# Kernel optimization log

Measured on AMD Instinct MI355X. Metric: run time of the kernel, lower is better.

Reference implementation:

```python
import jax, jax.numpy as jnp
import numpy as np

NUM_USERS = 50000
NUM_ITEMS = 50000
N = NUM_USERS + NUM_ITEMS
EMBED_K = 64
N_LAYERS = 3
FEAT = 2048
N_EDGES = 2000000
BATCH = 8192
LEAKY_SLOPE = 0.2


def _l2norm(x):
    # torch F.normalize(p=2, dim=1): x / max(||x||, 1e-12)
    return x / jnp.maximum(jnp.linalg.norm(x, axis=1, keepdims=True), 1e-12)


def setup_inputs():
    key = jax.random.key(0)
    ks = jax.random.split(key, 12)
    s = 1.0 / np.sqrt(EMBED_K)
    return {
        "Gu": jax.random.normal(ks[0], (NUM_USERS, EMBED_K), jnp.float32) * 0.1,
        "Gi": jax.random.normal(ks[1], (NUM_ITEMS, EMBED_K), jnp.float32) * 0.1,
        "Tu": jax.random.normal(ks[2], (NUM_USERS, EMBED_K), jnp.float32) * 0.1,
        "F": jax.random.uniform(ks[3], (NUM_ITEMS, FEAT), jnp.float32),
        "proj_w": jax.random.normal(ks[4], (EMBED_K, FEAT), jnp.float32) / np.sqrt(FEAT),
        "proj_b": jnp.zeros((EMBED_K,), jnp.float32),
        "W1": jax.random.normal(ks[5], (N_LAYERS, EMBED_K, EMBED_K), jnp.float32) * s,
        "b1": jnp.zeros((N_LAYERS, EMBED_K), jnp.float32),
        "W2": jax.random.normal(ks[6], (N_LAYERS, EMBED_K, EMBED_K), jnp.float32) * s,
        "b2": jnp.zeros((N_LAYERS, EMBED_K), jnp.float32),
        "edge_weight": jax.random.uniform(ks[7], (N_EDGES,), jnp.float32) * 0.05,
        "edge_index": jax.random.randint(ks[8], (2, N_EDGES), 0, N, jnp.int32),
        "users": jax.random.randint(ks[9], (BATCH,), 0, NUM_USERS, jnp.int32),
        "items": jax.random.randint(ks[10], (BATCH,), 0, NUM_ITEMS, jnp.int32),
    }


def _propagate(Gu, Gi, W1, b1, W2, b2, edge_weight, edge_index):
    src, dst = edge_index[0], edge_index[1]
    x = jnp.concatenate([Gu, Gi], axis=0)  # [N, d]
    embs = [x]
    for l in range(N_LAYERS):
        # sparse adjacency aggregation: agg = A_hat @ x
        msg = x[src] * edge_weight[:, None]              # [E, d]
        agg = jax.ops.segment_sum(msg, dst, num_segments=N)  # [N, d]
        # NGCF layer: W1(x + agg) + W2(x * agg), leaky relu
        h = (x + agg) @ W1[l].T + b1[l] + (x * agg) @ W2[l].T + b2[l]
        h = jax.nn.leaky_relu(h, LEAKY_SLOPE)
        # dropout p=0 (identity), then per-node L2 normalize
        h = _l2norm(h)
        embs.append(h)
        x = h
    all_e = jnp.mean(jnp.stack(embs, axis=1), axis=1)  # mean over layers
    return all_e[:NUM_USERS], all_e[NUM_USERS:]


def reference(Gu, Gi, Tu, F, proj_w, proj_b, W1, b1, W2, b2, edge_weight, edge_index, users, items):
    gu, gi = _propagate(Gu, Gi, W1, b1, W2, b2, edge_weight, edge_index)
    gamma_u = gu[users]          # [B, d]
    gamma_i = gi[items]          # [B, d]
    theta_u = Tu[users]          # [B, d]
    proj_i = _l2norm(F[items] @ proj_w.T + proj_b)  # [B, d]
    xui = jnp.sum(gamma_u * gamma_i, axis=1) + jnp.sum(theta_u * proj_i, axis=1)
    return xui
```

## Files before the change

kernel.cpp:

```cpp
#include <hip/hip_runtime.h>

#define NUSERS 50000
#define NITEMS 50000
#define NN (NUSERS + NITEMS)
#define KDIM 64
#define NLAYERS 3
#define FEAT 2048
#define NEDGES 2000000
#define BATCH 8192
#define SLOPE 0.2f

#define BSLOT 64
#define CNT_PAD 100352
#define XBLK 6250
#define CBLK 98
#define TBLK 128
#define NNK (NN * KDIM)
#define PROJ_BLOCKS (BATCH / 16)
#define FILL_BLOCKS ((NEDGES + 511) / 512)

typedef __attribute__((ext_vector_type(8))) short bf16x8;
typedef __attribute__((ext_vector_type(4))) float f32x4;

union U8 {
    bf16x8 v;
    uint4 u;
};

__device__ __forceinline__ unsigned short f2bf(float f) {
    unsigned int u = __float_as_uint(f);
    unsigned int r = (u + 0x7fffu + ((u >> 16) & 1u)) >> 16;
    return (unsigned short)r;
}
__device__ __forceinline__ unsigned int pack2(float a, float b) {
    return (unsigned int)f2bf(a) | ((unsigned int)f2bf(b) << 16);
}
__device__ __forceinline__ float b2f(unsigned short h) {
    return __uint_as_float((unsigned int)h << 16);
}

__global__ __launch_bounds__(256) void setup_kernel(const float* __restrict__ Gu,
                                                    const float* __restrict__ Gi,
                                                    const float* __restrict__ pw,
                                                    unsigned short* __restrict__ xh,
                                                    int* __restrict__ cnt,
                                                    unsigned short* __restrict__ pwh) {
    int bx = blockIdx.x;
    if (bx < XBLK) {
        int i = bx * 256 + threadIdx.x;
        const int totalU = NUSERS * KDIM / 4;
        float4 v = (i < totalU) ? ((const float4*)Gu)[i] : ((const float4*)Gi)[i - totalU];
        ushort4 h;
        h.x = f2bf(v.x); h.y = f2bf(v.y); h.z = f2bf(v.z); h.w = f2bf(v.w);
        ((ushort4*)xh)[i] = h;
    } else if (bx < XBLK + CBLK) {
        int i = (bx - XBLK) * 256 + threadIdx.x;
        ((int4*)cnt)[i] = make_int4(0, 0, 0, 0);
    } else {
        int i = (bx - XBLK - CBLK) * 256 + threadIdx.x;
        float4 v = ((const float4*)pw)[i];
        ushort4 h;
        h.x = f2bf(v.x); h.y = f2bf(v.y); h.z = f2bf(v.z); h.w = f2bf(v.w);
        ((ushort4*)pwh)[i] = h;
    }
}

__global__ __launch_bounds__(512) void proj_fill_kernel(const float* __restrict__ F,
                                                        const unsigned short* __restrict__ pwh,
                                                        const float* __restrict__ pb,
                                                        const int* __restrict__ items,
                                                        float* __restrict__ projB,
                                                        const int* __restrict__ ei,
                                                        const float* __restrict__ ew,
                                                        int* __restrict__ cnt,
                                                        unsigned int* __restrict__ bucket) {
    __shared__ float lds[8][64][16];
    int t = threadIdx.x;
    if (blockIdx.x >= PROJ_BLOCKS) {
        int e = (blockIdx.x - PROJ_BLOCKS) * 512 + t;
        if (e < NEDGES) {
            int src = ei[e];
            int dst = ei[NEDGES + e];
            int slot = atomicAdd(&cnt[dst], 1);
            if (slot < BSLOT)
                bucket[((long long)dst << 6) + slot] =
                    ((unsigned int)src << 15) | ((unsigned int)f2bf(ew[e]) & 0x7FFFu);
        }
        return;
    }
    int l = t & 63, w = t >> 6, m16 = l & 15, g4 = l >> 4;
    int i0 = blockIdx.x * 16;
    int item = items[i0 + m16];
    const float* frow = F + (long long)item * FEAT + g4 * 8;
    f32x4 acc[4];
#pragma unroll
    for (int c = 0; c < 4; ++c) acc[c] = (f32x4){0.f, 0.f, 0.f, 0.f};
    float4 fa[8], fb[8];
#pragma unroll
    for (int u = 0; u < 8; ++u) {
        const float* p = frow + (w * 8 + u) * 32;
        fa[u] = *(const float4*)p;
        fb[u] = *(const float4*)(p + 4);
    }
#pragma unroll
    for (int u = 0; u < 8; ++u) {
        U8 af;
        af.u = make_uint4(pack2(fa[u].x, fa[u].y), pack2(fa[u].z, fa[u].w),
                          pack2(fb[u].x, fb[u].y), pack2(fb[u].z, fb[u].w));
#pragma unroll
        for (int c = 0; c < 4; ++c) {
            bf16x8 bw = *(const bf16x8*)(pwh + (long long)(c * 16 + m16) * FEAT +
                                         (w * 8 + u) * 32 + g4 * 8);
            acc[c] = __builtin_amdgcn_mfma_f32_16x16x32_bf16(af.v, bw, acc[c], 0, 0, 0);
        }
    }
#pragma unroll
    for (int c = 0; c < 4; ++c)
#pragma unroll
        for (int reg = 0; reg < 4; ++reg) lds[w][l][c * 4 + reg] = acc[c][reg];
    __syncthreads();
    for (int e = t; e < 1024; e += 512) {
        int ll = e >> 4, v = e & 15;
        float s = lds[0][ll][v];
#pragma unroll
        for (int ww = 1; ww < 8; ++ww) s += lds[ww][ll][v];
        lds[0][ll][v] = s;
    }
    __syncthreads();
    if (w == 0) {
        float av[4][4];
        float sq[4] = {0.f, 0.f, 0.f, 0.f};
#pragma unroll
        for (int c = 0; c < 4; ++c) {
            float bb = pb[c * 16 + m16];
#pragma unroll
            for (int reg = 0; reg < 4; ++reg) {
                float h = lds[0][l][c * 4 + reg] + bb;
                av[c][reg] = h;
                sq[reg] += h * h;
            }
        }
#pragma unroll
        for (int reg = 0; reg < 4; ++reg) {
#pragma unroll
            for (int off = 1; off < 16; off <<= 1) sq[reg] += __shfl_xor(sq[reg], off);
            sq[reg] = 1.0f / fmaxf(sqrtf(sq[reg]), 1e-12f);
        }
#pragma unroll
        for (int reg = 0; reg < 4; ++reg) {
            int b = i0 + g4 * 4 + reg;
#pragma unroll
            for (int c = 0; c < 4; ++c)
                projB[(long long)b * KDIM + c * 16 + m16] = av[c][reg] * sq[reg];
        }
    }
}

__global__ __launch_bounds__(256) void agg_kernel(const unsigned short* __restrict__ xh,
                                                  const unsigned int* __restrict__ bucket,
                                                  const int* __restrict__ cnt,
                                                  unsigned short* __restrict__ aggh) {
    int t = threadIdx.x;
    int lane = t & 63, wid = t >> 6;
    int g = lane >> 3, l8 = lane & 7;
    int n = (blockIdx.x * 4 + wid) * 8 + g;
    if (n >= NN) return;
    int m = cnt[n];
    if (m > BSLOT) m = BSLOT;
    const unsigned int* bk = bucket + ((long long)n << 6);
    const uint4* x4 = (const uint4*)xh;
    float a0[8], a1[8], a2[8], a3[8];
#pragma unroll
    for (int q = 0; q < 8; ++q) { a0[q] = 0.f; a1[q] = 0.f; a2[q] = 0.f; a3[q] = 0.f; }
    int j = 0;
    for (; j + 4 <= m; j += 4) {
        unsigned int p0 = bk[j], p1 = bk[j + 1], p2 = bk[j + 2], p3 = bk[j + 3];
        uint4 u0 = x4[((long long)(p0 >> 15) << 3) + l8];
        uint4 u1 = x4[((long long)(p1 >> 15) << 3) + l8];
        uint4 u2 = x4[((long long)(p2 >> 15) << 3) + l8];
        uint4 u3 = x4[((long long)(p3 >> 15) << 3) + l8];
        float w0 = __uint_as_float((p0 & 0x7FFFu) << 16);
        float w1 = __uint_as_float((p1 & 0x7FFFu) << 16);
        float w2 = __uint_as_float((p2 & 0x7FFFu) << 16);
        float w3 = __uint_as_float((p3 & 0x7FFFu) << 16);
        a0[0] += w0 * __uint_as_float(u0.x << 16); a0[1] += w0 * __uint_as_float(u0.x & 0xFFFF0000u);
        a0[2] += w0 * __uint_as_float(u0.y << 16); a0[3] += w0 * __uint_as_float(u0.y & 0xFFFF0000u);
        a0[4] += w0 * __uint_as_float(u0.z << 16); a0[5] += w0 * __uint_as_float(u0.z & 0xFFFF0000u);
        a0[6] += w0 * __uint_as_float(u0.w << 16); a0[7] += w0 * __uint_as_float(u0.w & 0xFFFF0000u);
        a1[0] += w1 * __uint_as_float(u1.x << 16); a1[1] += w1 * __uint_as_float(u1.x & 0xFFFF0000u);
        a1[2] += w1 * __uint_as_float(u1.y << 16); a1[3] += w1 * __uint_as_float(u1.y & 0xFFFF0000u);
        a1[4] += w1 * __uint_as_float(u1.z << 16); a1[5] += w1 * __uint_as_float(u1.z & 0xFFFF0000u);
        a1[6] += w1 * __uint_as_float(u1.w << 16); a1[7] += w1 * __uint_as_float(u1.w & 0xFFFF0000u);
        a2[0] += w2 * __uint_as_float(u2.x << 16); a2[1] += w2 * __uint_as_float(u2.x & 0xFFFF0000u);
        a2[2] += w2 * __uint_as_float(u2.y << 16); a2[3] += w2 * __uint_as_float(u2.y & 0xFFFF0000u);
        a2[4] += w2 * __uint_as_float(u2.z << 16); a2[5] += w2 * __uint_as_float(u2.z & 0xFFFF0000u);
        a2[6] += w2 * __uint_as_float(u2.w << 16); a2[7] += w2 * __uint_as_float(u2.w & 0xFFFF0000u);
        a3[0] += w3 * __uint_as_float(u3.x << 16); a3[1] += w3 * __uint_as_float(u3.x & 0xFFFF0000u);
        a3[2] += w3 * __uint_as_float(u3.y << 16); a3[3] += w3 * __uint_as_float(u3.y & 0xFFFF0000u);
        a3[4] += w3 * __uint_as_float(u3.z << 16); a3[5] += w3 * __uint_as_float(u3.z & 0xFFFF0000u);
        a3[6] += w3 * __uint_as_float(u3.w << 16); a3[7] += w3 * __uint_as_float(u3.w & 0xFFFF0000u);
    }
    for (; j < m; ++j) {
        unsigned int p0 = bk[j];
        uint4 u0 = x4[((long long)(p0 >> 15) << 3) + l8];
        float w0 = __uint_as_float((p0 & 0x7FFFu) << 16);
        a0[0] += w0 * __uint_as_float(u0.x << 16); a0[1] += w0 * __uint_as_float(u0.x & 0xFFFF0000u);
        a0[2] += w0 * __uint_as_float(u0.y << 16); a0[3] += w0 * __uint_as_float(u0.y & 0xFFFF0000u);
        a0[4] += w0 * __uint_as_float(u0.z << 16); a0[5] += w0 * __uint_as_float(u0.z & 0xFFFF0000u);
        a0[6] += w0 * __uint_as_float(u0.w << 16); a0[7] += w0 * __uint_as_float(u0.w & 0xFFFF0000u);
    }
#pragma unroll
    for (int q = 0; q < 8; ++q) a0[q] = (a0[q] + a1[q]) + (a2[q] + a3[q]);
    uint4 o;
    o.x = pack2(a0[0], a0[1]); o.y = pack2(a0[2], a0[3]);
    o.z = pack2(a0[4], a0[5]); o.w = pack2(a0[6], a0[7]);
    *(uint4*)(aggh + (long long)n * KDIM + l8 * 8) = o;
}

__global__ __launch_bounds__(256) void gemm_layer_kernel(const unsigned short* __restrict__ xh_in,
                                                         const unsigned short* __restrict__ aggh,
                                                         const float* __restrict__ W1,
                                                         const float* __restrict__ b1,
                                                         const float* __restrict__ W2,
                                                         const float* __restrict__ b2,
                                                         unsigned short* __restrict__ xhout,
                                                         int layer) {
    __shared__ unsigned short sS[64 * 72];
    __shared__ unsigned short sP[64 * 72];
    __shared__ unsigned short sW1[64 * 72];
    __shared__ unsigned short sW2[64 * 72];
    int t = threadIdx.x;
    const float* W1g = W1 + (long long)layer * KDIM * KDIM;
    const float* W2g = W2 + (long long)layer * KDIM * KDIM;
    for (int idx = t; idx < KDIM * KDIM; idx += 256) {
        int j = idx >> 6, k = idx & 63;
        sW1[j * 72 + k] = f2bf(W1g[idx]);
        sW2[j * 72 + k] = f2bf(W2g[idx]);
    }
    int n0 = blockIdx.x * 64;
    {
        int r = t >> 2, q = t & 3;
        int node = n0 + r;
        unsigned short* dS = &sS[r * 72 + q * 16];
        unsigned short* dP = &sP[r * 72 + q * 16];
        if (node < NN) {
            const unsigned short* xb = xh_in + (long long)node * KDIM + q * 16;
            const unsigned short* ab = aggh + (long long)node * KDIM + q * 16;
            uint4 hx = *(const uint4*)xb;
            uint4 hx2 = *(const uint4*)(xb + 8);
            uint4 ha = *(const uint4*)ab;
            uint4 ha2 = *(const uint4*)(ab + 8);
            uint4 swv, pwv, swv2, pwv2;
#define PROC(XW, AW, SW, PW)                                                        \
            {                                                                       \
                float xx0 = __uint_as_float((XW) << 16);                            \
                float xx1 = __uint_as_float((XW) & 0xFFFF0000u);                    \
                float aa0 = __uint_as_float((AW) << 16);                            \
                float aa1 = __uint_as_float((AW) & 0xFFFF0000u);                    \
                SW = pack2(xx0 + aa0, xx1 + aa1);                                   \
                PW = pack2(xx0 * aa0, xx1 * aa1);                                   \
            }
            PROC(hx.x, ha.x, swv.x, pwv.x)
            PROC(hx.y, ha.y, swv.y, pwv.y)
            PROC(hx.z, ha.z, swv.z, pwv.z)
            PROC(hx.w, ha.w, swv.w, pwv.w)
            PROC(hx2.x, ha2.x, swv2.x, pwv2.x)
            PROC(hx2.y, ha2.y, swv2.y, pwv2.y)
            PROC(hx2.z, ha2.z, swv2.z, pwv2.z)
            PROC(hx2.w, ha2.w, swv2.w, pwv2.w)
#undef PROC
            *(uint4*)dS = swv;
            *(uint4*)(dS + 8) = swv2;
            *(uint4*)dP = pwv;
            *(uint4*)(dP + 8) = pwv2;
        } else {
            uint4 z = make_uint4(0, 0, 0, 0);
            *(uint4*)dS = z; *(uint4*)(dS + 8) = z;
            *(uint4*)dP = z; *(uint4*)(dP + 8) = z;
        }
    }
    __syncthreads();

    int l = t & 63, w = t >> 6, m16 = l & 15, g4 = l >> 4;
    f32x4 acc[4];
#pragma unroll
    for (int c = 0; c < 4; ++c) {
        float bb = b1[layer * KDIM + c * 16 + m16] + b2[layer * KDIM + c * 16 + m16];
        acc[c] = (f32x4){bb, bb, bb, bb};
    }
    const int abase = (w * 16 + m16) * 72;
#pragma unroll
    for (int kh = 0; kh < 2; ++kh) {
        int ko = kh * 32 + g4 * 8;
        bf16x8 aS = *(const bf16x8*)&sS[abase + ko];
        bf16x8 aP = *(const bf16x8*)&sP[abase + ko];
#pragma unroll
        for (int c = 0; c < 4; ++c) {
            bf16x8 bw1 = *(const bf16x8*)&sW1[(c * 16 + m16) * 72 + ko];
            acc[c] = __builtin_amdgcn_mfma_f32_16x16x32_bf16(aS, bw1, acc[c], 0, 0, 0);
            bf16x8 bw2 = *(const bf16x8*)&sW2[(c * 16 + m16) * 72 + ko];
            acc[c] = __builtin_amdgcn_mfma_f32_16x16x32_bf16(aP, bw2, acc[c], 0, 0, 0);
        }
    }

    float sq[4] = {0.f, 0.f, 0.f, 0.f};
#pragma unroll
    for (int c = 0; c < 4; ++c) {
#pragma unroll
        for (int reg = 0; reg < 4; ++reg) {
            float h = acc[c][reg];
            h = h > 0.f ? h : SLOPE * h;
            acc[c][reg] = h;
            sq[reg] += h * h;
        }
    }
#pragma unroll
    for (int reg = 0; reg < 4; ++reg) {
#pragma unroll
        for (int off = 1; off < 16; off <<= 1) sq[reg] += __shfl_xor(sq[reg], off);
        sq[reg] = 1.0f / fmaxf(sqrtf(sq[reg]), 1e-12f);
    }
#pragma unroll
    for (int reg = 0; reg < 4; ++reg) {
        int node = n0 + w * 16 + g4 * 4 + reg;
        if (node < NN) {
#pragma unroll
            for (int c = 0; c < 4; ++c)
                xhout[(long long)node * KDIM + c * 16 + m16] = f2bf(acc[c][reg] * sq[reg]);
        }
    }
}

__global__ __launch_bounds__(256) void final_kernel(const unsigned short* __restrict__ xh0,
                                                    const unsigned short* __restrict__ xh1,
                                                    const unsigned short* __restrict__ xh2,
                                                    const unsigned short* __restrict__ xh3,
                                                    const float* __restrict__ Tu,
                                                    const float* __restrict__ projB,
                                                    const int* __restrict__ users,
                                                    const int* __restrict__ items,
                                                    float* __restrict__ out) {
    int lane = threadIdx.x & 63;
    int wid = threadIdx.x >> 6;
    int b = blockIdx.x * 4 + wid;
    if (b >= BATCH) return;
    int u = users[b];
    int it = NUSERS + items[b];
    long long uo = (long long)u * KDIM + lane;
    long long io = (long long)it * KDIM + lane;
    float gu = b2f(xh0[uo]) + b2f(xh1[uo]) + b2f(xh2[uo]) + b2f(xh3[uo]);
    float gi = b2f(xh0[io]) + b2f(xh1[io]) + b2f(xh2[io]) + b2f(xh3[io]);
    float tu = Tu[(long long)u * KDIM + lane];
    float pi = projB[(long long)b * KDIM + lane];
    float v = gu * gi * (1.0f / 16.0f) + tu * pi;
#pragma unroll
    for (int off = 32; off > 0; off >>= 1) v += __shfl_xor(v, off);
    if (lane == 0) out[b] = v;
}

extern "C" void kernel_launch(void* const* d_in, const int* in_sizes, int n_in,
                              void* d_out, int out_size, void* d_ws, size_t ws_size,
                              hipStream_t stream) {
    const float* Gu = (const float*)d_in[0];
    const float* Gi = (const float*)d_in[1];
    const float* Tu = (const float*)d_in[2];
    const float* F = (const float*)d_in[3];
    const float* pw = (const float*)d_in[4];
    const float* pb = (const float*)d_in[5];
    const float* W1 = (const float*)d_in[6];
    const float* b1 = (const float*)d_in[7];
    const float* W2 = (const float*)d_in[8];
    const float* b2 = (const float*)d_in[9];
    const float* ew = (const float*)d_in[10];
    const int* ei = (const int*)d_in[11];
    const int* users = (const int*)d_in[12];
    const int* items = (const int*)d_in[13];
    float* out = (float*)d_out;

    float* projB = (float*)d_ws;
    unsigned int* bucket = (unsigned int*)(projB + (size_t)BATCH * KDIM);
    int* cnt = (int*)(bucket + (size_t)NN * BSLOT);
    unsigned short* aggh = (unsigned short*)(cnt + CNT_PAD);
    unsigned short* pwh = aggh + (size_t)NNK;
    unsigned short* xh0 = pwh + (size_t)KDIM * FEAT;
    unsigned short* xh1 = xh0 + (size_t)NNK;
    unsigned short* xh2 = xh1 + (size_t)NNK;
    unsigned short* xh3 = xh2 + (size_t)NNK;

    setup_kernel<<<XBLK + CBLK + TBLK, 256, 0, stream>>>(Gu, Gi, pw, xh0, cnt, pwh);
    proj_fill_kernel<<<PROJ_BLOCKS + FILL_BLOCKS, 512, 0, stream>>>(F, pwh, pb, items, projB,
                                                                    ei, ew, cnt, bucket);

    unsigned short* xs[4] = {xh0, xh1, xh2, xh3};
    for (int ll = 0; ll < NLAYERS; ++ll) {
        agg_kernel<<<(NN + 31) / 32, 256, 0, stream>>>(xs[ll], bucket, cnt, aggh);
        gemm_layer_kernel<<<(NN + 63) / 64, 256, 0, stream>>>(xs[ll], aggh, W1, b1, W2, b2,
                                                              xs[ll + 1], ll);
    }

    final_kernel<<<BATCH / 4, 256, 0, stream>>>(xh0, xh1, xh2, xh3, Tu, projB, users, items, out);
}
```

Measured before the change: 333.8 us.

## Fuse sparse aggregation with NGCF layer GEMM and pre-convert weights to bf16

Merges agg_kernel and gemm_layer_kernel into one per-layer kernel. Each lane gathers neighbour rows directly into the MFMA A-operand layout (node per m16, k-slice per g4), so the intermediate aggregate buffer is no longer written to and re-read from global memory, and two launches per layer are removed. W1/W2 are converted to bf16 once in the setup kernel and read from global memory instead of being staged through LDS in every block. The trade-off is a less contiguous gather (each lane loads two 16-byte chunks per neighbour) and divergence from differing node degrees within a wave.

```diff
diff --git a/kernel.cpp b/kernel.cpp
--- a/kernel.cpp
+++ b/kernel.cpp
@@ -15,6 +15,7 @@
 #define XBLK 6250
 #define CBLK 98
 #define TBLK 128
+#define W4BLK 12
 #define NNK (NN * KDIM)
 #define PROJ_BLOCKS (BATCH / 16)
 #define FILL_BLOCKS ((NEDGES + 511) / 512)
@@ -39,12 +40,39 @@
     return __uint_as_float((unsigned int)h << 16);
 }
 
+#define ACC8(A, W, U)                                   \
+    A[0] += (W) * __uint_as_float((U).x << 16);         \
+    A[1] += (W) * __uint_as_float((U).x & 0xFFFF0000u); \
+    A[2] += (W) * __uint_as_float((U).y << 16);         \
+    A[3] += (W) * __uint_as_float((U).y & 0xFFFF0000u); \
+    A[4] += (W) * __uint_as_float((U).z << 16);         \
+    A[5] += (W) * __uint_as_float((U).z & 0xFFFF0000u); \
+    A[6] += (W) * __uint_as_float((U).w << 16);         \
+    A[7] += (W) * __uint_as_float((U).w & 0xFFFF0000u);
+
+#define MKSP(XV, A, SU, PU)                                                          \
+    {                                                                                \
+        float x0, x1;                                                                \
+        x0 = __uint_as_float((XV).x << 16); x1 = __uint_as_float((XV).x & 0xFFFF0000u); \
+        (SU).x = pack2(x0 + (A)[0], x1 + (A)[1]); (PU).x = pack2(x0 * (A)[0], x1 * (A)[1]); \
+        x0 = __uint_as_float((XV).y << 16); x1 = __uint_as_float((XV).y & 0xFFFF0000u); \
+        (SU).y = pack2(x0 + (A)[2], x1 + (A)[3]); (PU).y = pack2(x0 * (A)[2], x1 * (A)[3]); \
+        x0 = __uint_as_float((XV).z << 16); x1 = __uint_as_float((XV).z & 0xFFFF0000u); \
+        (SU).z = pack2(x0 + (A)[4], x1 + (A)[5]); (PU).z = pack2(x0 * (A)[4], x1 * (A)[5]); \
+        x0 = __uint_as_float((XV).w << 16); x1 = __uint_as_float((XV).w & 0xFFFF0000u); \
+        (SU).w = pack2(x0 + (A)[6], x1 + (A)[7]); (PU).w = pack2(x0 * (A)[6], x1 * (A)[7]); \
+    }
+
 __global__ __launch_bounds__(256) void setup_kernel(const float* __restrict__ Gu,
                                                     const float* __restrict__ Gi,
                                                     const float* __restrict__ pw,
+                                                    const float* __restrict__ W1,
+                                                    const float* __restrict__ W2,
                                                     unsigned short* __restrict__ xh,
                                                     int* __restrict__ cnt,
-                                                    unsigned short* __restrict__ pwh) {
+                                                    unsigned short* __restrict__ pwh,
+                                                    unsigned short* __restrict__ w1h,
+                                                    unsigned short* __restrict__ w2h) {
     int bx = blockIdx.x;
     if (bx < XBLK) {
         int i = bx * 256 + threadIdx.x;
@@ -56,12 +84,21 @@
     } else if (bx < XBLK + CBLK) {
         int i = (bx - XBLK) * 256 + threadIdx.x;
         ((int4*)cnt)[i] = make_int4(0, 0, 0, 0);
-    } else {
+    } else if (bx < XBLK + CBLK + TBLK) {
         int i = (bx - XBLK - CBLK) * 256 + threadIdx.x;
         float4 v = ((const float4*)pw)[i];
         ushort4 h;
         h.x = f2bf(v.x); h.y = f2bf(v.y); h.z = f2bf(v.z); h.w = f2bf(v.w);
         ((ushort4*)pwh)[i] = h;
+    } else {
+        int b2x = bx - XBLK - CBLK - TBLK;
+        const float* srcw = (b2x < W4BLK) ? W1 : W2;
+        unsigned short* dstw = (b2x < W4BLK) ? w1h : w2h;
+        int i = (b2x % W4BLK) * 256 + threadIdx.x;
+        float4 v = ((const float4*)srcw)[i];
+        ushort4 h;
+        h.x = f2bf(v.x); h.y = f2bf(v.y); h.z = f2bf(v.z); h.w = f2bf(v.w);
+        ((ushort4*)dstw)[i] = h;
     }
 }
 
@@ -156,151 +193,82 @@
     }
 }
 
-__global__ __launch_bounds__(256) void agg_kernel(const unsigned short* __restrict__ xh,
-                                                  const unsigned int* __restrict__ bucket,
-                                                  const int* __restrict__ cnt,
-                                                  unsigned short* __restrict__ aggh) {
+__global__ __launch_bounds__(256) void layer_fused_kernel(const unsigned short* __restrict__ xh_in,
+                                                          const unsigned int* __restrict__ bucket,
+                                                          const int* __restrict__ cnt,
+                                                          const unsigned short* __restrict__ w1h,
+                                                          const unsigned short* __restrict__ w2h,
+                                                          const float* __restrict__ b1,
+                                                          const float* __restrict__ b2,
+                                                          unsigned short* __restrict__ xhout,
+                                                          int layer) {
     int t = threadIdx.x;
-    int lane = t & 63, wid = t >> 6;
-    int g = lane >> 3, l8 = lane & 7;
-    int n = (blockIdx.x * 4 + wid) * 8 + g;
-    if (n >= NN) return;
-    int m = cnt[n];
+    int l = t & 63, w = t >> 6;
+    int m16 = l & 15, g4 = l >> 4;
+    int node = blockIdx.x * 64 + w * 16 + m16;
+    int ok = node < NN;
+    int nc = ok ? node : 0;
+    int m = ok ? cnt[nc] : 0;
     if (m > BSLOT) m = BSLOT;
-    const unsigned int* bk = bucket + ((long long)n << 6);
-    const uint4* x4 = (const uint4*)xh;
-    float a0[8], a1[8], a2[8], a3[8];
-#pragma unroll
-    for (int q = 0; q < 8; ++q) { a0[q] = 0.f; a1[q] = 0.f; a2[q] = 0.f; a3[q] = 0.f; }
+    const unsigned int* bk = bucket + ((long long)nc << 6);
+    const uint4* x4 = (const uint4*)xh_in;
+
+    float a0l[8], a0h[8], a1l[8], a1h[8];
+#pragma unroll
+    for (int q = 0; q < 8; ++q) { a0l[q] = 0.f; a0h[q] = 0.f; a1l[q] = 0.f; a1h[q] = 0.f; }
     int j = 0;
-    for (; j + 4 <= m; j += 4) {
-        unsigned int p0 = bk[j], p1 = bk[j + 1], p2 = bk[j + 2], p3 = bk[j + 3];
-        uint4 u0 = x4[((long long)(p0 >> 15) << 3) + l8];
-        uint4 u1 = x4[((long long)(p1 >> 15) << 3) + l8];
-        uint4 u2 = x4[((long long)(p2 >> 15) << 3) + l8];
-        uint4 u3 = x4[((long long)(p3 >> 15) << 3) + l8];
+    for (; j + 2 <= m; j += 2) {
+        unsigned int p0 = bk[j], p1 = bk[j + 1];
+        long long r0 = (long long)(p0 >> 15) << 3;
+        long long r1 = (long long)(p1 >> 15) << 3;
+        uint4 u0l = x4[r0 + g4];
+        uint4 u0h = x4[r0 + 4 + g4];
+        uint4 u1l = x4[r1 + g4];
+        uint4 u1h = x4[r1 + 4 + g4];
         float w0 = __uint_as_float((p0 & 0x7FFFu) << 16);
         float w1 = __uint_as_float((p1 & 0x7FFFu) << 16);
-        float w2 = __uint_as_float((p2 & 0x7FFFu) << 16);
-        float w3 = __uint_as_float((p3 & 0x7FFFu) << 16);
-        a0[0] += w0 * __uint_as_float(u0.x << 16); a0[1] += w0 * __uint_as_float(u0.x & 0xFFFF0000u);
-        a0[2] += w0 * __uint_as_float(u0.y << 16); a0[3] += w0 * __uint_as_float(u0.y & 0xFFFF0000u);
-        a0[4] += w0 * __uint_as_float(u0.z << 16); a0[5] += w0 * __uint_as_float(u0.z & 0xFFFF0000u);
-        a0[6] += w0 * __uint_as_float(u0.w << 16); a0[7] += w0 * __uint_as_float(u0.w & 0xFFFF0000u);
-        a1[0] += w1 * __uint_as_float(u1.x << 16); a1[1] += w1 * __uint_as_float(u1.x & 0xFFFF0000u);
-        a1[2] += w1 * __uint_as_float(u1.y << 16); a1[3] += w1 * __uint_as_float(u1.y & 0xFFFF0000u);
-        a1[4] += w1 * __uint_as_float(u1.z << 16); a1[5] += w1 * __uint_as_float(u1.z & 0xFFFF0000u);
-        a1[6] += w1 * __uint_as_float(u1.w << 16); a1[7] += w1 * __uint_as_float(u1.w & 0xFFFF0000u);
-        a2[0] += w2 * __uint_as_float(u2.x << 16); a2[1] += w2 * __uint_as_float(u2.x & 0xFFFF0000u);
-        a2[2] += w2 * __uint_as_float(u2.y << 16); a2[3] += w2 * __uint_as_float(u2.y & 0xFFFF0000u);
-        a2[4] += w2 * __uint_as_float(u2.z << 16); a2[5] += w2 * __uint_as_float(u2.z & 0xFFFF0000u);
-        a2[6] += w2 * __uint_as_float(u2.w << 16); a2[7] += w2 * __uint_as_float(u2.w & 0xFFFF0000u);
-        a3[0] += w3 * __uint_as_float(u3.x << 16); a3[1] += w3 * __uint_as_float(u3.x & 0xFFFF0000u);
-        a3[2] += w3 * __uint_as_float(u3.y << 16); a3[3] += w3 * __uint_as_float(u3.y & 0xFFFF0000u);
-        a3[4] += w3 * __uint_as_float(u3.z << 16); a3[5] += w3 * __uint_as_float(u3.z & 0xFFFF0000u);
-        a3[6] += w3 * __uint_as_float(u3.w << 16); a3[7] += w3 * __uint_as_float(u3.w & 0xFFFF0000u);
-    }
-    for (; j < m; ++j) {
+        ACC8(a0l, w0, u0l)
+        ACC8(a0h, w0, u0h)
+        ACC8(a1l, w1, u1l)
+        ACC8(a1h, w1, u1h)
+    }
+    if (j < m) {
         unsigned int p0 = bk[j];
-        uint4 u0 = x4[((long long)(p0 >> 15) << 3) + l8];
+        long long r0 = (long long)(p0 >> 15) << 3;
+        uint4 u0l = x4[r0 + g4];
+        uint4 u0h = x4[r0 + 4 + g4];
         float w0 = __uint_as_float((p0 & 0x7FFFu) << 16);
-        a0[0] += w0 * __uint_as_float(u0.x << 16); a0[1] += w0 * __uint_as_float(u0.x & 0xFFFF0000u);
-        a0[2] += w0 * __uint_as_float(u0.y << 16); a0[3] += w0 * __uint_as_float(u0.y & 0xFFFF0000u);
-        a0[4] += w0 * __uint_as_float(u0.z << 16); a0[5] += w0 * __uint_as_float(u0.z & 0xFFFF0000u);
-        a0[6] += w0 * __uint_as_float(u0.w << 16); a0[7] += w0 * __uint_as_float(u0.w & 0xFFFF0000u);
-    }
-#pragma unroll
-    for (int q = 0; q < 8; ++q) a0[q] = (a0[q] + a1[q]) + (a2[q] + a3[q]);
-    uint4 o;
-    o.x = pack2(a0[0], a0[1]); o.y = pack2(a0[2], a0[3]);
-    o.z = pack2(a0[4], a0[5]); o.w = pack2(a0[6], a0[7]);
-    *(uint4*)(aggh + (long long)n * KDIM + l8 * 8) = o;
-}
-
-__global__ __launch_bounds__(256) void gemm_layer_kernel(const unsigned short* __restrict__ xh_in,
-                                                         const unsigned short* __restrict__ aggh,
-                                                         const float* __restrict__ W1,
-                                                         const float* __restrict__ b1,
-                                                         const float* __restrict__ W2,
-                                                         const float* __restrict__ b2,
-                                                         unsigned short* __restrict__ xhout,
-                                                         int layer) {
-    __shared__ unsigned short sS[64 * 72];
-    __shared__ unsigned short sP[64 * 72];
-    __shared__ unsigned short sW1[64 * 72];
-    __shared__ unsigned short sW2[64 * 72];
-    int t = threadIdx.x;
-    const float* W1g = W1 + (long long)layer * KDIM * KDIM;
-    const float* W2g = W2 + (long long)layer * KDIM * KDIM;
-    for (int idx = t; idx < KDIM * KDIM; idx += 256) {
-        int j = idx >> 6, k = idx & 63;
-        sW1[j * 72 + k] = f2bf(W1g[idx]);
-        sW2[j * 72 + k] = f2bf(W2g[idx]);
-    }
-    int n0 = blockIdx.x * 64;
-    {
-        int r = t >> 2, q = t & 3;
-        int node = n0 + r;
-        unsigned short* dS = &sS[r * 72 + q * 16];
-        unsigned short* dP = &sP[r * 72 + q * 16];
-        if (node < NN) {
-            const unsigned short* xb = xh_in + (long long)node * KDIM + q * 16;
-            const unsigned short* ab = aggh + (long long)node * KDIM + q * 16;
-            uint4 hx = *(const uint4*)xb;
-            uint4 hx2 = *(const uint4*)(xb + 8);
-            uint4 ha = *(const uint4*)ab;
-            uint4 ha2 = *(const uint4*)(ab + 8);
-            uint4 swv, pwv, swv2, pwv2;
-#define PROC(XW, AW, SW, PW)                                                        \
-            {                                                                       \
-                float xx0 = __uint_as_float((XW) << 16);                            \
-                float xx1 = __uint_as_float((XW) & 0xFFFF0000u);                    \
-                float aa0 = __uint_as_float((AW) << 16);                            \
-                float aa1 = __uint_as_float((AW) & 0xFFFF0000u);                    \
-                SW = pack2(xx0 + aa0, xx1 + aa1);                                   \
-                PW = pack2(xx0 * aa0, xx1 * aa1);                                   \
-            }
-            PROC(hx.x, ha.x, swv.x, pwv.x)
-            PROC(hx.y, ha.y, swv.y, pwv.y)
-            PROC(hx.z, ha.z, swv.z, pwv.z)
-            PROC(hx.w, ha.w, swv.w, pwv.w)
-            PROC(hx2.x, ha2.x, swv2.x, pwv2.x)
-            PROC(hx2.y, ha2.y, swv2.y, pwv2.y)
-            PROC(hx2.z, ha2.z, swv2.z, pwv2.z)
-            PROC(hx2.w, ha2.w, swv2.w, pwv2.w)
-#undef PROC
-            *(uint4*)dS = swv;
-            *(uint4*)(dS + 8) = swv2;
-            *(uint4*)dP = pwv;
-            *(uint4*)(dP + 8) = pwv2;
-        } else {
-            uint4 z = make_uint4(0, 0, 0, 0);
-            *(uint4*)dS = z; *(uint4*)(dS + 8) = z;
-            *(uint4*)dP = z; *(uint4*)(dP + 8) = z;
-        }
-    }
-    __syncthreads();
-
-    int l = t & 63, w = t >> 6, m16 = l & 15, g4 = l >> 4;
+        ACC8(a0l, w0, u0l)
+        ACC8(a0h, w0, u0h)
+    }
+#pragma unroll
+    for (int q = 0; q < 8; ++q) { a0l[q] += a1l[q]; a0h[q] += a1h[q]; }
+
+    uint4 xvl = x4[((long long)nc << 3) + g4];
+    uint4 xvh = x4[((long long)nc << 3) + 4 + g4];
+    U8 s0, p0f, s1, p1f;
+    MKSP(xvl, a0l, s0.u, p0f.u)
+    MKSP(xvh, a0h, s1.u, p1f.u)
+
     f32x4 acc[4];
 #pragma unroll
     for (int c = 0; c < 4; ++c) {
         float bb = b1[layer * KDIM + c * 16 + m16] + b2[layer * KDIM + c * 16 + m16];
         acc[c] = (f32x4){bb, bb, bb, bb};
     }
-    const int abase = (w * 16 + m16) * 72;
-#pragma unroll
-    for (int kh = 0; kh < 2; ++kh) {
-        int ko = kh * 32 + g4 * 8;
-        bf16x8 aS = *(const bf16x8*)&sS[abase + ko];
-        bf16x8 aP = *(const bf16x8*)&sP[abase + ko];
-#pragma unroll
-        for (int c = 0; c < 4; ++c) {
-            bf16x8 bw1 = *(const bf16x8*)&sW1[(c * 16 + m16) * 72 + ko];
-            acc[c] = __builtin_amdgcn_mfma_f32_16x16x32_bf16(aS, bw1, acc[c], 0, 0, 0);
-            bf16x8 bw2 = *(const bf16x8*)&sW2[(c * 16 + m16) * 72 + ko];
-            acc[c] = __builtin_amdgcn_mfma_f32_16x16x32_bf16(aP, bw2, acc[c], 0, 0, 0);
-        }
+    const unsigned short* w1l = w1h + (long long)layer * KDIM * KDIM;
+    const unsigned short* w2l = w2h + (long long)layer * KDIM * KDIM;
+#pragma unroll
+    for (int c = 0; c < 4; ++c) {
+        int nrow = (c * 16 + m16) * KDIM;
+        bf16x8 b10 = *(const bf16x8*)&w1l[nrow + g4 * 8];
+        acc[c] = __builtin_amdgcn_mfma_f32_16x16x32_bf16(s0.v, b10, acc[c], 0, 0, 0);
+        bf16x8 b20 = *(const bf16x8*)&w2l[nrow + g4 * 8];
+        acc[c] = __builtin_amdgcn_mfma_f32_16x16x32_bf16(p0f.v, b20, acc[c], 0, 0, 0);
+        bf16x8 b11 = *(const bf16x8*)&w1l[nrow + 32 + g4 * 8];
+        acc[c] = __builtin_amdgcn_mfma_f32_16x16x32_bf16(s1.v, b11, acc[c], 0, 0, 0);
+        bf16x8 b21 = *(const bf16x8*)&w2l[nrow + 32 + g4 * 8];
+        acc[c] = __builtin_amdgcn_mfma_f32_16x16x32_bf16(p1f.v, b21, acc[c], 0, 0, 0);
     }
 
     float sq[4] = {0.f, 0.f, 0.f, 0.f};
@@ -320,13 +288,14 @@
         for (int off = 1; off < 16; off <<= 1) sq[reg] += __shfl_xor(sq[reg], off);
         sq[reg] = 1.0f / fmaxf(sqrtf(sq[reg]), 1e-12f);
     }
+    int nb = blockIdx.x * 64 + w * 16;
 #pragma unroll
     for (int reg = 0; reg < 4; ++reg) {
-        int node = n0 + w * 16 + g4 * 4 + reg;
-        if (node < NN) {
+        int onode = nb + g4 * 4 + reg;
+        if (onode < NN) {
 #pragma unroll
             for (int c = 0; c < 4; ++c)
-                xhout[(long long)node * KDIM + c * 16 + m16] = f2bf(acc[c][reg] * sq[reg]);
+                xhout[(long long)onode * KDIM + c * 16 + m16] = f2bf(acc[c][reg] * sq[reg]);
         }
     }
 }
@@ -380,22 +349,23 @@
     float* projB = (float*)d_ws;
     unsigned int* bucket = (unsigned int*)(projB + (size_t)BATCH * KDIM);
     int* cnt = (int*)(bucket + (size_t)NN * BSLOT);
-    unsigned short* aggh = (unsigned short*)(cnt + CNT_PAD);
-    unsigned short* pwh = aggh + (size_t)NNK;
-    unsigned short* xh0 = pwh + (size_t)KDIM * FEAT;
+    unsigned short* pwh = (unsigned short*)(cnt + CNT_PAD);
+    unsigned short* w1h = pwh + (size_t)KDIM * FEAT;
+    unsigned short* w2h = w1h + (size_t)NLAYERS * KDIM * KDIM;
+    unsigned short* xh0 = w2h + (size_t)NLAYERS * KDIM * KDIM;
     unsigned short* xh1 = xh0 + (size_t)NNK;
     unsigned short* xh2 = xh1 + (size_t)NNK;
     unsigned short* xh3 = xh2 + (size_t)NNK;
 
-    setup_kernel<<<XBLK + CBLK + TBLK, 256, 0, stream>>>(Gu, Gi, pw, xh0, cnt, pwh);
+    setup_kernel<<<XBLK + CBLK + TBLK + 2 * W4BLK, 256, 0, stream>>>(Gu, Gi, pw, W1, W2, xh0,
+                                                                     cnt, pwh, w1h, w2h);
     proj_fill_kernel<<<PROJ_BLOCKS + FILL_BLOCKS, 512, 0, stream>>>(F, pwh, pb, items, projB,
                                                                     ei, ew, cnt, bucket);
 
     unsigned short* xs[4] = {xh0, xh1, xh2, xh3};
     for (int ll = 0; ll < NLAYERS; ++ll) {
-        agg_kernel<<<(NN + 31) / 32, 256, 0, stream>>>(xs[ll], bucket, cnt, aggh);
-        gemm_layer_kernel<<<(NN + 63) / 64, 256, 0, stream>>>(xs[ll], aggh, W1, b1, W2, b2,
-                                                              xs[ll + 1], ll);
+        layer_fused_kernel<<<(NN + 63) / 64, 256, 0, stream>>>(xs[ll], bucket, cnt, w1h, w2h,
+                                                               b1, b2, xs[ll + 1], ll);
     }
 
     final_kernel<<<BATCH / 4, 256, 0, stream>>>(xh0, xh1, xh2, xh3, Tu, projB, users, items, out);
```

Measured after the change: 375.6 us. +12.5%, slower.

## Split embeddings into four 16-column planes and gather per plane in aggregation

Applied to the files above, without the earlier changes.

Node embeddings and aggregation buffers move from row-major [N,64] to four column-quarter planes of [N,16]. The aggregation kernel runs four passes over nodes, one per plane, so each gather touches a 3.2 MB plane instead of the full 12.8 MB table, which is meant to improve cache hit rates for random neighbour reads. It also marks bucket reads as nontemporal. The cost is four times as many bucket reads and gather instructions, each only 32 bits wide, and the GEMM, setup and final kernels must index the new layout.

```diff
diff --git a/kernel.cpp b/kernel.cpp
--- a/kernel.cpp
+++ b/kernel.cpp
@@ -18,6 +18,7 @@
 #define NNK (NN * KDIM)
 #define PROJ_BLOCKS (BATCH / 16)
 #define FILL_BLOCKS ((NEDGES + 511) / 512)
+#define AGG_PB ((NN + 31) / 32)
 
 typedef __attribute__((ext_vector_type(8))) short bf16x8;
 typedef __attribute__((ext_vector_type(4))) float f32x4;
@@ -42,7 +43,7 @@
 __global__ __launch_bounds__(256) void setup_kernel(const float* __restrict__ Gu,
                                                     const float* __restrict__ Gi,
                                                     const float* __restrict__ pw,
-                                                    unsigned short* __restrict__ xh,
+                                                    unsigned short* __restrict__ xt,
                                                     int* __restrict__ cnt,
                                                     unsigned short* __restrict__ pwh) {
     int bx = blockIdx.x;
@@ -52,7 +53,9 @@
         float4 v = (i < totalU) ? ((const float4*)Gu)[i] : ((const float4*)Gi)[i - totalU];
         ushort4 h;
         h.x = f2bf(v.x); h.y = f2bf(v.y); h.z = f2bf(v.z); h.w = f2bf(v.w);
-        ((ushort4*)xh)[i] = h;
+        int n = i >> 4, s = i & 15;
+        int q = s >> 2, s4 = s & 3;
+        *(ushort4*)(xt + ((size_t)(q * NN + n) << 4) + s4 * 4) = h;
     } else if (bx < XBLK + CBLK) {
         int i = (bx - XBLK) * 256 + threadIdx.x;
         ((int4*)cnt)[i] = make_int4(0, 0, 0, 0);
@@ -156,74 +159,59 @@
     }
 }
 
-__global__ __launch_bounds__(256) void agg_kernel(const unsigned short* __restrict__ xh,
+__global__ __launch_bounds__(256) void agg_kernel(const unsigned short* __restrict__ xt,
                                                   const unsigned int* __restrict__ bucket,
                                                   const int* __restrict__ cnt,
-                                                  unsigned short* __restrict__ aggh) {
+                                                  unsigned short* __restrict__ aggt) {
     int t = threadIdx.x;
     int lane = t & 63, wid = t >> 6;
     int g = lane >> 3, l8 = lane & 7;
-    int n = (blockIdx.x * 4 + wid) * 8 + g;
+    int p = blockIdx.x / AGG_PB;
+    int n = ((blockIdx.x % AGG_PB) * 4 + wid) * 8 + g;
     if (n >= NN) return;
     int m = cnt[n];
     if (m > BSLOT) m = BSLOT;
     const unsigned int* bk = bucket + ((long long)n << 6);
-    const uint4* x4 = (const uint4*)xh;
-    float a0[8], a1[8], a2[8], a3[8];
-#pragma unroll
-    for (int q = 0; q < 8; ++q) { a0[q] = 0.f; a1[q] = 0.f; a2[q] = 0.f; a3[q] = 0.f; }
+    const unsigned int* xs = (const unsigned int*)(xt + ((size_t)p * NN << 4)) + l8;
+    float a0[2], a1[2], a2[2], a3[2];
+    a0[0] = a0[1] = a1[0] = a1[1] = a2[0] = a2[1] = a3[0] = a3[1] = 0.f;
     int j = 0;
     for (; j + 4 <= m; j += 4) {
-        unsigned int p0 = bk[j], p1 = bk[j + 1], p2 = bk[j + 2], p3 = bk[j + 3];
-        uint4 u0 = x4[((long long)(p0 >> 15) << 3) + l8];
-        uint4 u1 = x4[((long long)(p1 >> 15) << 3) + l8];
-        uint4 u2 = x4[((long long)(p2 >> 15) << 3) + l8];
-        uint4 u3 = x4[((long long)(p3 >> 15) << 3) + l8];
+        unsigned int p0 = __builtin_nontemporal_load(bk + j);
+        unsigned int p1 = __builtin_nontemporal_load(bk + j + 1);
+        unsigned int p2 = __builtin_nontemporal_load(bk + j + 2);
+        unsigned int p3 = __builtin_nontemporal_load(bk + j + 3);
+        unsigned int u0 = xs[(size_t)(p0 >> 15) << 3];
+        unsigned int u1 = xs[(size_t)(p1 >> 15) << 3];
+        unsigned int u2 = xs[(size_t)(p2 >> 15) << 3];
+        unsigned int u3 = xs[(size_t)(p3 >> 15) << 3];
         float w0 = __uint_as_float((p0 & 0x7FFFu) << 16);
         float w1 = __uint_as_float((p1 & 0x7FFFu) << 16);
         float w2 = __uint_as_float((p2 & 0x7FFFu) << 16);
         float w3 = __uint_as_float((p3 & 0x7FFFu) << 16);
-        a0[0] += w0 * __uint_as_float(u0.x << 16); a0[1] += w0 * __uint_as_float(u0.x & 0xFFFF0000u);
-        a0[2] += w0 * __uint_as_float(u0.y << 16); a0[3] += w0 * __uint_as_float(u0.y & 0xFFFF0000u);
-        a0[4] += w0 * __uint_as_float(u0.z << 16); a0[5] += w0 * __uint_as_float(u0.z & 0xFFFF0000u);
-        a0[6] += w0 * __uint_as_float(u0.w << 16); a0[7] += w0 * __uint_as_float(u0.w & 0xFFFF0000u);
-        a1[0] += w1 * __uint_as_float(u1.x << 16); a1[1] += w1 * __uint_as_float(u1.x & 0xFFFF0000u);
-        a1[2] += w1 * __uint_as_float(u1.y << 16); a1[3] += w1 * __uint_as_float(u1.y & 0xFFFF0000u);
-        a1[4] += w1 * __uint_as_float(u1.z << 16); a1[5] += w1 * __uint_as_float(u1.z & 0xFFFF0000u);
-        a1[6] += w1 * __uint_as_float(u1.w << 16); a1[7] += w1 * __uint_as_float(u1.w & 0xFFFF0000u);
-        a2[0] += w2 * __uint_as_float(u2.x << 16); a2[1] += w2 * __uint_as_float(u2.x & 0xFFFF0000u);
-        a2[2] += w2 * __uint_as_float(u2.y << 16); a2[3] += w2 * __uint_as_float(u2.y & 0xFFFF0000u);
-        a2[4] += w2 * __uint_as_float(u2.z << 16); a2[5] += w2 * __uint_as_float(u2.z & 0xFFFF0000u);
-        a2[6] += w2 * __uint_as_float(u2.w << 16); a2[7] += w2 * __uint_as_float(u2.w & 0xFFFF0000u);
-        a3[0] += w3 * __uint_as_float(u3.x << 16); a3[1] += w3 * __uint_as_float(u3.x & 0xFFFF0000u);
-        a3[2] += w3 * __uint_as_float(u3.y << 16); a3[3] += w3 * __uint_as_float(u3.y & 0xFFFF0000u);
-        a3[4] += w3 * __uint_as_float(u3.z << 16); a3[5] += w3 * __uint_as_float(u3.z & 0xFFFF0000u);
-        a3[6] += w3 * __uint_as_float(u3.w << 16); a3[7] += w3 * __uint_as_float(u3.w & 0xFFFF0000u);
+        a0[0] += w0 * __uint_as_float(u0 << 16); a0[1] += w0 * __uint_as_float(u0 & 0xFFFF0000u);
+        a1[0] += w1 * __uint_as_float(u1 << 16); a1[1] += w1 * __uint_as_float(u1 & 0xFFFF0000u);
+        a2[0] += w2 * __uint_as_float(u2 << 16); a2[1] += w2 * __uint_as_float(u2 & 0xFFFF0000u);
+        a3[0] += w3 * __uint_as_float(u3 << 16); a3[1] += w3 * __uint_as_float(u3 & 0xFFFF0000u);
     }
     for (; j < m; ++j) {
-        unsigned int p0 = bk[j];
-        uint4 u0 = x4[((long long)(p0 >> 15) << 3) + l8];
+        unsigned int p0 = __builtin_nontemporal_load(bk + j);
+        unsigned int u0 = xs[(size_t)(p0 >> 15) << 3];
         float w0 = __uint_as_float((p0 & 0x7FFFu) << 16);
-        a0[0] += w0 * __uint_as_float(u0.x << 16); a0[1] += w0 * __uint_as_float(u0.x & 0xFFFF0000u);
-        a0[2] += w0 * __uint_as_float(u0.y << 16); a0[3] += w0 * __uint_as_float(u0.y & 0xFFFF0000u);
-        a0[4] += w0 * __uint_as_float(u0.z << 16); a0[5] += w0 * __uint_as_float(u0.z & 0xFFFF0000u);
-        a0[6] += w0 * __uint_as_float(u0.w << 16); a0[7] += w0 * __uint_as_float(u0.w & 0xFFFF0000u);
-    }
-#pragma unroll
-    for (int q = 0; q < 8; ++q) a0[q] = (a0[q] + a1[q]) + (a2[q] + a3[q]);
-    uint4 o;
-    o.x = pack2(a0[0], a0[1]); o.y = pack2(a0[2], a0[3]);
-    o.z = pack2(a0[4], a0[5]); o.w = pack2(a0[6], a0[7]);
-    *(uint4*)(aggh + (long long)n * KDIM + l8 * 8) = o;
-}
-
-__global__ __launch_bounds__(256) void gemm_layer_kernel(const unsigned short* __restrict__ xh_in,
-                                                         const unsigned short* __restrict__ aggh,
+        a0[0] += w0 * __uint_as_float(u0 << 16); a0[1] += w0 * __uint_as_float(u0 & 0xFFFF0000u);
+    }
+    float lo = (a0[0] + a1[0]) + (a2[0] + a3[0]);
+    float hi = (a0[1] + a1[1]) + (a2[1] + a3[1]);
+    *(unsigned int*)(aggt + ((size_t)(p * NN + n) << 4) + l8 * 2) = pack2(lo, hi);
+}
+
+__global__ __launch_bounds__(256) void gemm_layer_kernel(const unsigned short* __restrict__ xt_in,
+                                                         const unsigned short* __restrict__ aggt,
                                                          const float* __restrict__ W1,
                                                          const float* __restrict__ b1,
                                                          const float* __restrict__ W2,
                                                          const float* __restrict__ b2,
-                                                         unsigned short* __restrict__ xhout,
+                                                         unsigned short* __restrict__ xt_out,
                                                          int layer) {
     __shared__ unsigned short sS[64 * 72];
     __shared__ unsigned short sP[64 * 72];
@@ -244,8 +232,8 @@
         unsigned short* dS = &sS[r * 72 + q * 16];
         unsigned short* dP = &sP[r * 72 + q * 16];
         if (node < NN) {
-            const unsigned short* xb = xh_in + (long long)node * KDIM + q * 16;
-            const unsigned short* ab = aggh + (long long)node * KDIM + q * 16;
+            const unsigned short* xb = xt_in + ((size_t)(q * NN + node) << 4);
+            const unsigned short* ab = aggt + ((size_t)(q * NN + node) << 4);
             uint4 hx = *(const uint4*)xb;
             uint4 hx2 = *(const uint4*)(xb + 8);
             uint4 ha = *(const uint4*)ab;
@@ -326,15 +314,15 @@
         if (node < NN) {
 #pragma unroll
             for (int c = 0; c < 4; ++c)
-                xhout[(long long)node * KDIM + c * 16 + m16] = f2bf(acc[c][reg] * sq[reg]);
-        }
-    }
-}
-
-__global__ __launch_bounds__(256) void final_kernel(const unsigned short* __restrict__ xh0,
-                                                    const unsigned short* __restrict__ xh1,
-                                                    const unsigned short* __restrict__ xh2,
-                                                    const unsigned short* __restrict__ xh3,
+                xt_out[((size_t)(c * NN + node) << 4) + m16] = f2bf(acc[c][reg] * sq[reg]);
+        }
+    }
+}
+
+__global__ __launch_bounds__(256) void final_kernel(const unsigned short* __restrict__ xt0,
+                                                    const unsigned short* __restrict__ xt1,
+                                                    const unsigned short* __restrict__ xt2,
+                                                    const unsigned short* __restrict__ xt3,
                                                     const float* __restrict__ Tu,
                                                     const float* __restrict__ projB,
                                                     const int* __restrict__ users,
@@ -346,10 +334,11 @@
     if (b >= BATCH) return;
     int u = users[b];
     int it = NUSERS + items[b];
-    long long uo = (long long)u * KDIM + lane;
-    long long io = (long long)it * KDIM + lane;
-    float gu = b2f(xh0[uo]) + b2f(xh1[uo]) + b2f(xh2[uo]) + b2f(xh3[uo]);
-    float gi = b2f(xh0[io]) + b2f(xh1[io]) + b2f(xh2[io]) + b2f(xh3[io]);
+    int q = lane >> 4, d = lane & 15;
+    size_t uo = ((size_t)(q * NN + u) << 4) + d;
+    size_t io = ((size_t)(q * NN + it) << 4) + d;
+    float gu = b2f(xt0[uo]) + b2f(xt1[uo]) + b2f(xt2[uo]) + b2f(xt3[uo]);
+    float gi = b2f(xt0[io]) + b2f(xt1[io]) + b2f(xt2[io]) + b2f(xt3[io]);
     float tu = Tu[(long long)u * KDIM + lane];
     float pi = projB[(long long)b * KDIM + lane];
     float v = gu * gi * (1.0f / 16.0f) + tu * pi;
@@ -380,23 +369,23 @@
     float* projB = (float*)d_ws;
     unsigned int* bucket = (unsigned int*)(projB + (size_t)BATCH * KDIM);
     int* cnt = (int*)(bucket + (size_t)NN * BSLOT);
-    unsigned short* aggh = (unsigned short*)(cnt + CNT_PAD);
-    unsigned short* pwh = aggh + (size_t)NNK;
-    unsigned short* xh0 = pwh + (size_t)KDIM * FEAT;
-    unsigned short* xh1 = xh0 + (size_t)NNK;
-    unsigned short* xh2 = xh1 + (size_t)NNK;
-    unsigned short* xh3 = xh2 + (size_t)NNK;
-
-    setup_kernel<<<XBLK + CBLK + TBLK, 256, 0, stream>>>(Gu, Gi, pw, xh0, cnt, pwh);
+    unsigned short* aggt = (unsigned short*)(cnt + CNT_PAD);
+    unsigned short* pwh = aggt + (size_t)NNK;
+    unsigned short* xt0 = pwh + (size_t)KDIM * FEAT;
+    unsigned short* xt1 = xt0 + (size_t)NNK;
+    unsigned short* xt2 = xt1 + (size_t)NNK;
+    unsigned short* xt3 = xt2 + (size_t)NNK;
+
+    setup_kernel<<<XBLK + CBLK + TBLK, 256, 0, stream>>>(Gu, Gi, pw, xt0, cnt, pwh);
     proj_fill_kernel<<<PROJ_BLOCKS + FILL_BLOCKS, 512, 0, stream>>>(F, pwh, pb, items, projB,
                                                                     ei, ew, cnt, bucket);
 
-    unsigned short* xs[4] = {xh0, xh1, xh2, xh3};
+    unsigned short* xs[4] = {xt0, xt1, xt2, xt3};
     for (int ll = 0; ll < NLAYERS; ++ll) {
-        agg_kernel<<<(NN + 31) / 32, 256, 0, stream>>>(xs[ll], bucket, cnt, aggh);
-        gemm_layer_kernel<<<(NN + 63) / 64, 256, 0, stream>>>(xs[ll], aggh, W1, b1, W2, b2,
+        agg_kernel<<<4 * AGG_PB, 256, 0, stream>>>(xs[ll], bucket, cnt, aggt);
+        gemm_layer_kernel<<<(NN + 63) / 64, 256, 0, stream>>>(xs[ll], aggt, W1, b1, W2, b2,
                                                               xs[ll + 1], ll);
     }
 
-    final_kernel<<<BATCH / 4, 256, 0, stream>>>(xh0, xh1, xh2, xh3, Tu, projB, users, items, out);
-}
+    final_kernel<<<BATCH / 4, 256, 0, stream>>>(xt0, xt1, xt2, xt3, Tu, projB, users, items, out);
+}
```

Measured after the change: 507.7 us. +52.1%, slower.
